# Kernel tuning notes

Hardware: AMD Instinct MI355X
Metric: run time of the kernel (lower is better)

## Reference

```python
import jax, jax.numpy as jnp
import numpy as np

DIM = 2048
NUM_SLOTS = 64
MEM_DIM = 512
TEMP = 0.1


def setup_inputs() -> dict:
    key = jax.random.key(0)
    k_x, k_mem, k_kp, k_vp, k_gw, k_gb = jax.random.split(key, 6)
    B, L = 8, 4096
    return {
        "x": jax.random.normal(k_x, (B, L, DIM), dtype=jnp.float32),
        "memory": jax.random.normal(k_mem, (NUM_SLOTS, MEM_DIM), dtype=jnp.float32),
        # torch Linear weight layout: [out_features, in_features]
        "key_w": jax.random.normal(k_kp, (MEM_DIM, DIM), dtype=jnp.float32) * (1.0 / np.sqrt(DIM)),
        "value_w": jax.random.normal(k_vp, (DIM, MEM_DIM), dtype=jnp.float32) * (1.0 / np.sqrt(MEM_DIM)),
        "gate_w": jax.random.normal(k_gw, (1, 2 * DIM), dtype=jnp.float32) * (1.0 / np.sqrt(2 * DIM)),
        "gate_b": jnp.zeros((1,), dtype=jnp.float32),
    }


def reference(x, memory, key_w, value_w, gate_w, gate_b):
    # query = key_proj(x): [B,L,mem_dim]
    query = jnp.einsum('bld,md->blm', x, key_w)
    # attention over memory slots: [B,L,num_slots]
    attn = jax.nn.softmax(jnp.einsum('blm,nm->bln', query, memory) / TEMP, axis=-1)
    # retrieve and project back to dim: [B,L,dim]
    retrieved = jnp.einsum('bln,nm->blm', attn, memory)
    retrieved = jnp.einsum('blm,dm->bld', retrieved, value_w)
    # gate from concat([x, retrieved]) -> Linear(2*dim, 1) -> sigmoid
    gate_logit = (jnp.einsum('bld,od->blo', x, gate_w[:, :DIM])
                  + jnp.einsum('bld,od->blo', retrieved, gate_w[:, DIM:])
                  + gate_b)
    gate = jax.nn.sigmoid(gate_logit)  # [B,L,1]
    return gate * x + (1.0 - gate) * retrieved
```

## Files before the change

### kernel.cpp

```cpp
#include <hip/hip_runtime.h>
#include <stdint.h>

#define DIM   2048
#define NSLOT 64
#define MDIM  512
#define TINV  10.0f

typedef __attribute__((ext_vector_type(4))) float     f32x4;
typedef __attribute__((ext_vector_type(8))) _Float16  half8;

#define MFMA16(a,b,c) __builtin_amdgcn_mfma_f32_16x16x32_f16((a),(b),(c),0,0,0)

#define OFF_W2F   0
#define OFF_W3T   1310720
#define OFF_H     1572864
#define OFF_TPART 1573120

__device__ __forceinline__ size_t w2f_idx(int row, int k, int lvl) {
    const int t  = row >> 4, ar = row & 15;
    const int ch = k >> 7, ks = (k >> 5) & 3, kg = (k >> 3) & 3, e = k & 7;
    return ((size_t)((((ch * 5 + t) * 4 + ks) * 2 + lvl) * 64) + kg * 16 + ar) * 8 + e;
}


__global__ __launch_bounds__(256) void prep_all(
    const float* __restrict__ memory, const float* __restrict__ key_w,
    const float* __restrict__ value_w, const float* __restrict__ gate_w,
    _Float16* __restrict__ W2F, _Float16* __restrict__ W3T,
    float* __restrict__ tpart)
{
    const int tid = threadIdx.x;
    const int c = blockIdx.x;
    const int role = blockIdx.y;

    if (role == 17) {
        const int b = c;
        float a0 = 0.f, a1 = 0.f;
        for (int d = b * 256; d < b * 256 + 256; ++d) {
            const float gv = gate_w[DIM + d];
            a0 = fmaf(value_w[(size_t)d * MDIM + tid], gv, a0);
            a1 = fmaf(value_w[(size_t)d * MDIM + tid + 256], gv, a1);
        }
        tpart[b * 512 + tid] = a0;
        tpart[b * 512 + tid + 256] = a1;
        return;
    }

    if (role < 9) {
        const int g = role;
        const int k = c * 256 + tid;
        if (g == 8) {
            float v = gate_w[k];
            _Float16 ph = (_Float16)v;
            _Float16 pl = (_Float16)(v - (float)ph);
            W2F[w2f_idx(64, k, 0)] = ph;
            W2F[w2f_idx(64, k, 1)] = pl;
            for (int r = 65; r < 80; ++r) {
                W2F[w2f_idx(r, k, 0)] = (_Float16)0.f;
                W2F[w2f_idx(r, k, 1)] = (_Float16)0.f;
            }
            return;
        }
        __shared__ __align__(16) float mem_s[8 * MDIM];
        for (int i = tid; i < 8 * MDIM; i += 256)
            mem_s[i] = memory[g * 8 * MDIM + i];
        __syncthreads();

        const f32x4* ms4 = (const f32x4*)mem_s;
        float acc[8] = {};
        for (int m4 = 0; m4 < MDIM / 4; ++m4) {
            const float kw0 = key_w[(size_t)(m4 * 4 + 0) * DIM + k];
            const float kw1 = key_w[(size_t)(m4 * 4 + 1) * DIM + k];
            const float kw2 = key_w[(size_t)(m4 * 4 + 2) * DIM + k];
            const float kw3 = key_w[(size_t)(m4 * 4 + 3) * DIM + k];
            #pragma unroll
            for (int i = 0; i < 8; ++i) {
                const f32x4 mv = ms4[i * (MDIM / 4) + m4];
                acc[i] = fmaf(mv.x, kw0, acc[i]);
                acc[i] = fmaf(mv.y, kw1, acc[i]);
                acc[i] = fmaf(mv.z, kw2, acc[i]);
                acc[i] = fmaf(mv.w, kw3, acc[i]);
            }
        }
        #pragma unroll
        for (int i = 0; i < 8; ++i) {
            float v = acc[i];
            _Float16 ph = (_Float16)v;
            _Float16 pl = (_Float16)(v - (float)ph);
            W2F[w2f_idx(g * 8 + i, k, 0)] = ph;
            W2F[w2f_idx(g * 8 + i, k, 1)] = pl;
        }
        return;
    }

    {
        const int g = role - 9;
        const int d = c * 256 + tid;
        __shared__ __align__(16) float mem_s2[8 * MDIM];
        for (int i = tid; i < 8 * MDIM; i += 256)
            mem_s2[i] = memory[g * 8 * MDIM + i];
        __syncthreads();

        const f32x4* ms4 = (const f32x4*)mem_s2;
        const f32x4* vp = (const f32x4*)(value_w + (size_t)d * MDIM);
        float acc[8] = {};
        for (int m4 = 0; m4 < MDIM / 4; ++m4) {
            const f32x4 v = vp[m4];
            #pragma unroll
            for (int i = 0; i < 8; ++i) {
                const f32x4 mv = ms4[i * (MDIM / 4) + m4];
                acc[i] = fmaf(mv.x, v.x, acc[i]);
                acc[i] = fmaf(mv.y, v.y, acc[i]);
                acc[i] = fmaf(mv.z, v.z, acc[i]);
                acc[i] = fmaf(mv.w, v.w, acc[i]);
            }
        }
        #pragma unroll
        for (int i = 0; i < 8; ++i)
            W3T[(size_t)d * NSLOT + g * 8 + i] = (_Float16)acc[i];
    }
}

__global__ __launch_bounds__(512) void prep_h(
    const float* __restrict__ memory, const float* __restrict__ tpart,
    float* __restrict__ h)
{
    __shared__ float ts[512];
    const int tid = threadIdx.x;
    float s = 0.f;
    #pragma unroll
    for (int b = 0; b < 8; ++b) s += tpart[b * 512 + tid];
    ts[tid] = s;
    __syncthreads();
    const int lane = tid & 63, w = tid >> 6;
    #pragma unroll
    for (int q = 0; q < 8; ++q) {
        const int n = w * 8 + q;
        float p = 0.f;
        for (int m = lane; m < MDIM; m += 64)
            p = fmaf(memory[(size_t)n * MDIM + m], ts[m], p);
        #pragma unroll
        for (int off = 32; off; off >>= 1) p += __shfl_xor(p, off);
        if (lane == 0) h[n] = p;
    }
}


__global__ __launch_bounds__(512, 4) void fused_kernel(
    const float* __restrict__ x,
    const _Float16* __restrict__ W2F,
    const _Float16* __restrict__ W3T,
    const float* __restrict__ h, const float* __restrict__ gate_b,
    float* __restrict__ out)
{
    __shared__ __align__(16) float ppart[4 * 5 * 64 * 4];
    __shared__ __align__(16) _Float16 attn_s[4][16][72];
    __shared__ float gate_s[4][16];

    const int tid  = threadIdx.x;
    const int lane = tid & 63;
    const int w    = tid >> 6;
    const int mt   = w & 3;
    const int kh   = w >> 2;
    const int arow = lane & 15;
    const int kg   = lane >> 4;
    const size_t row0 = (size_t)blockIdx.x * 64;

    f32x4 acc[5];
    {   f32x4 z = {0.f, 0.f, 0.f, 0.f};
        #pragma unroll
        for (int t = 0; t < 5; ++t) acc[t] = z; }

    const float* xrow = x + (row0 + mt * 16 + arow) * DIM + kg * 8;
    const _Float16* w2l8 = W2F + lane * 8;
    const int chbase = kh * 8;

    f32x4 xA[8], xB[8];
    auto load_x = [&](f32x4* X, int chn) {
        #pragma unroll
        for (int ks = 0; ks < 4; ++ks) {
            X[ks * 2]     = *(const f32x4*)(xrow + chn * 128 + ks * 32);
            X[ks * 2 + 1] = *(const f32x4*)(xrow + chn * 128 + ks * 32 + 4);
        }
    };
    auto compute_chunk = [&](const f32x4* X, int ch) {
        #pragma unroll
        for (int ks = 0; ks < 4; ++ks) {
            const f32x4 xa = X[ks * 2];
            const f32x4 xb = X[ks * 2 + 1];
            const float xf[8] = {xa.x, xa.y, xa.z, xa.w, xb.x, xb.y, xb.z, xb.w};
            _Float16 hh[8], ll[8];
            #pragma unroll
            for (int u = 0; u < 8; ++u) {
                hh[u] = (_Float16)xf[u];
                ll[u] = (_Float16)(xf[u] - (float)hh[u]);
            }
            const half8 ah = {hh[0], hh[1], hh[2], hh[3], hh[4], hh[5], hh[6], hh[7]};
            const half8 al = {ll[0], ll[1], ll[2], ll[3], ll[4], ll[5], ll[6], ll[7]};
            #pragma unroll
            for (int t = 0; t < 5; ++t) {
                const _Float16* p = w2l8 + (size_t)(((ch * 5 + t) * 4 + ks) * 2) * 512;
                const half8 bh = *(const half8*)p;
                const half8 bl = *(const half8*)(p + 512);
                acc[t] = MFMA16(ah, bh, acc[t]);
                acc[t] = MFMA16(al, bh, acc[t]);
                acc[t] = MFMA16(ah, bl, acc[t]);
            }
        }
    };

    load_x(xA, chbase);
    for (int cp = 0; cp < 8; cp += 2) {
        load_x(xB, chbase + cp + 1);
        compute_chunk(xA, chbase + cp);
        if (cp + 2 < 8) load_x(xA, chbase + cp + 2);
        compute_chunk(xB, chbase + cp + 1);
    }

    if (kh == 1) {
        #pragma unroll
        for (int t = 0; t < 5; ++t)
            *(f32x4*)(ppart + (size_t)((mt * 5 + t) * 64 + lane) * 4) = acc[t];
    }
    __syncthreads();

    if (kh == 0) {
        #pragma unroll
        for (int t = 0; t < 5; ++t)
            acc[t] += *(const f32x4*)(ppart + (size_t)((mt * 5 + t) * 64 + lane) * 4);

        float hl[4];
        #pragma unroll
        for (int t = 0; t < 4; ++t) hl[t] = h[t * 16 + arow];
        const float gb = gate_b[0];

        #pragma unroll
        for (int j = 0; j < 4; ++j) {
            float m = fmaxf(fmaxf(acc[0][j], acc[1][j]), fmaxf(acc[2][j], acc[3][j]));
            #pragma unroll
            for (int off = 1; off < 16; off <<= 1) m = fmaxf(m, __shfl_xor(m, off));
            float p[4];
            float sum = 0.f;
            #pragma unroll
            for (int t = 0; t < 4; ++t) { p[t] = __expf((acc[t][j] - m) * TINV); sum += p[t]; }
            #pragma unroll
            for (int off = 1; off < 16; off <<= 1) sum += __shfl_xor(sum, off);
            const float inv = 1.f / sum;
            float gp = 0.f;
            #pragma unroll
            for (int t = 0; t < 4; ++t) {
                const float a = p[t] * inv;
                attn_s[mt][kg * 4 + j][t * 16 + arow] = (_Float16)a;
                gp = fmaf(a, hl[t], gp);
            }
            #pragma unroll
            for (int off = 1; off < 16; off <<= 1) gp += __shfl_xor(gp, off);
            const float sg = __shfl(acc[4][j], lane & 48);
            if (arow == 0)
                gate_s[mt][kg * 4 + j] = 1.f / (1.f + __expf(-(sg + gp + gb)));
        }
    }
    __syncthreads();

    const size_t rbase = row0 + mt * 16;
    const half8 a0 = *(const half8*)(&attn_s[mt][arow][kg * 8]);
    const half8 a1 = *(const half8*)(&attn_s[mt][arow][kg * 8 + 32]);
    const float g = gate_s[mt][arow];

    const size_t rowoff = (rbase + arow) * DIM + kh * 1024 + kg * 4;
    const float* xp = x + rowoff;
    float* op = out + rowoff;
    const _Float16* w3base = W3T + (size_t)(kh * 1024 + arow) * NSLOT + kg * 8;

    half8 qb0[4], qb1[4];
    f32x4 qx[4];
    #pragma unroll
    for (int s = 0; s < 4; ++s) {
        const _Float16* bp = w3base + (size_t)s * 16 * NSLOT;
        qb0[s] = *(const half8*)bp;
        qb1[s] = *(const half8*)(bp + 32);
        qx[s]  = *(const f32x4*)(xp + s * 16);
    }

    #pragma unroll 4
    for (int dt = 0; dt < 64; ++dt) {
        const int s = dt & 3;
        f32x4 r = {0.f, 0.f, 0.f, 0.f};
        r = MFMA16(qb0[s], a0, r);
        r = MFMA16(qb1[s], a1, r);
        const f32x4 xv = qx[s];
        int nt = dt + 4; if (nt > 63) nt = 63;
        const _Float16* bp = w3base + (size_t)nt * 16 * NSLOT;
        qb0[s] = *(const half8*)bp;
        qb1[s] = *(const half8*)(bp + 32);
        qx[s]  = *(const f32x4*)(xp + (size_t)nt * 16);
        f32x4 o;
        o.x = fmaf(g, xv.x - r.x, r.x);
        o.y = fmaf(g, xv.y - r.y, r.y);
        o.z = fmaf(g, xv.z - r.z, r.z);
        o.w = fmaf(g, xv.w - r.w, r.w);
        *(f32x4*)(op + dt * 16) = o;
    }
}


extern "C" void kernel_launch(void* const* d_in, const int* in_sizes, int n_in,
                              void* d_out, int out_size, void* d_ws, size_t ws_size,
                              hipStream_t stream) {
    (void)in_sizes; (void)n_in; (void)out_size; (void)ws_size;
    const float* x       = (const float*)d_in[0];
    const float* memory  = (const float*)d_in[1];
    const float* key_w   = (const float*)d_in[2];
    const float* value_w = (const float*)d_in[3];
    const float* gate_w  = (const float*)d_in[4];
    const float* gate_b  = (const float*)d_in[5];
    float* out = (float*)d_out;

    char* wsb = (char*)d_ws;
    _Float16* W2F = (_Float16*)(wsb + OFF_W2F);
    _Float16* W3T = (_Float16*)(wsb + OFF_W3T);
    float*    h   = (float*)(wsb + OFF_H);
    float*    tpt = (float*)(wsb + OFF_TPART);

    prep_all<<<dim3(8, 18), 256, 0, stream>>>(memory, key_w, value_w, gate_w,
                                              W2F, W3T, tpt);
    prep_h  <<<1, 512, 0, stream>>>(memory, tpt, h);

    fused_kernel<<<512, 512, 0, stream>>>(x, W2F, W3T, h, gate_b, out);
}
```

Baseline: 301.5 us.

## Stage 16-row x panel in LDS via direct global-to-LDS loads and reuse it

The fused kernel now processes 16 rows per 256-thread block. It copies the whole 16x2048 fp32 x panel into swizzled LDS with global_load_lds, then reuses that panel for the key projection, the gate dot product with x, and the final blend, with output staged in LDS and written out coalesced. This removes the second global read of x and the fifth (gate) MFMA tile from the projection. The catch is 128KB of LDS per block, which limits occupancy to roughly one block per CU, and a four-way K split that needs a cross-warp reduction.

```diff
diff --git a/kernel.cpp b/kernel.cpp
--- a/kernel.cpp
+++ b/kernel.cpp
@@ -10,6 +10,8 @@
 typedef __attribute__((ext_vector_type(8))) _Float16  half8;
 
 #define MFMA16(a,b,c) __builtin_amdgcn_mfma_f32_16x16x32_f16((a),(b),(c),0,0,0)
+#define AS1 __attribute__((address_space(1)))
+#define AS3 __attribute__((address_space(3)))
 
 #define OFF_W2F   0
 #define OFF_W3T   1310720
@@ -18,8 +20,9 @@
 
 __device__ __forceinline__ size_t w2f_idx(int row, int k, int lvl) {
     const int t  = row >> 4, ar = row & 15;
-    const int ch = k >> 7, ks = (k >> 5) & 3, kg = (k >> 3) & 3, e = k & 7;
-    return ((size_t)((((ch * 5 + t) * 4 + ks) * 2 + lvl) * 64) + kg * 16 + ar) * 8 + e;
+    const int ch = k >> 6, ks = (k >> 5) & 1, kg = (k >> 3) & 3, e = k & 7;
+    return (size_t)ch * 12288 +
+           ((size_t)(((t * 2 + ks) * 2 + lvl) * 64) + kg * 16 + ar) * 8 + e;
 }
 
 
@@ -146,92 +149,119 @@
 }
 
 
-__global__ __launch_bounds__(512, 4) void fused_kernel(
+__global__ __launch_bounds__(256) void fused_kernel(
     const float* __restrict__ x,
     const _Float16* __restrict__ W2F,
     const _Float16* __restrict__ W3T,
-    const float* __restrict__ h, const float* __restrict__ gate_b,
-    float* __restrict__ out)
+    const float* __restrict__ h, const float* __restrict__ gate_w,
+    const float* __restrict__ gate_b, float* __restrict__ out)
 {
-    __shared__ __align__(16) float ppart[4 * 5 * 64 * 4];
-    __shared__ __align__(16) _Float16 attn_s[4][16][72];
-    __shared__ float gate_s[4][16];
+    __shared__ __align__(16) float panel[16 * 2048];
+    __shared__ __align__(16) float ppart[3 * 4 * 64 * 4];
+    __shared__ __align__(16) _Float16 attn_s[16][72];
+    __shared__ float xg[16];
+    __shared__ float gate_s[16];
 
     const int tid  = threadIdx.x;
     const int lane = tid & 63;
     const int w    = tid >> 6;
-    const int mt   = w & 3;
-    const int kh   = w >> 2;
-    const int arow = lane & 15;
+    const int ar   = lane & 15;
     const int kg   = lane >> 4;
-    const size_t row0 = (size_t)blockIdx.x * 64;
-
-    f32x4 acc[5];
+    const size_t row0 = (size_t)blockIdx.x * 16;
+
+    #pragma unroll
+    for (int i = 0; i < 32; ++i) {
+        const int g   = i * 256 + tid;
+        const int row = g >> 9, q = g & 511;
+        const int lq  = q ^ (row & 7);
+        const char* src = (const char*)x + (row0 + row) * 8192 + (size_t)lq * 16;
+        float* dst = panel + (size_t)(i * 256 + w * 64) * 4;
+        __builtin_amdgcn_global_load_lds((const AS1 void*)src, (AS3 void*)dst, 16, 0, 0);
+    }
+    asm volatile("s_waitcnt vmcnt(0)" ::: "memory");
+    __builtin_amdgcn_s_barrier();
+
+    #pragma unroll
+    for (int rr = 0; rr < 4; ++rr) {
+        const int r = w * 4 + rr;
+        float a = 0.f;
+        #pragma unroll
+        for (int j = 0; j < 32; ++j) {
+            const int d = j * 64 + lane;
+            const float f = panel[r * 2048 + (((d >> 2) ^ (r & 7)) << 2) + (d & 3)];
+            a = fmaf(f, gate_w[d], a);
+        }
+        #pragma unroll
+        for (int off = 32; off; off >>= 1) a += __shfl_xor(a, off);
+        if (lane == 0) xg[r] = a;
+    }
+
+    f32x4 acc[4];
     {   f32x4 z = {0.f, 0.f, 0.f, 0.f};
         #pragma unroll
-        for (int t = 0; t < 5; ++t) acc[t] = z; }
-
-    const float* xrow = x + (row0 + mt * 16 + arow) * DIM + kg * 8;
-    const _Float16* w2l8 = W2F + lane * 8;
-    const int chbase = kh * 8;
-
-    f32x4 xA[8], xB[8];
-    auto load_x = [&](f32x4* X, int chn) {
-        #pragma unroll
-        for (int ks = 0; ks < 4; ++ks) {
-            X[ks * 2]     = *(const f32x4*)(xrow + chn * 128 + ks * 32);
-            X[ks * 2 + 1] = *(const f32x4*)(xrow + chn * 128 + ks * 32 + 4);
-        }
+        for (int t = 0; t < 4; ++t) acc[t] = z; }
+
+    const _Float16* w2base = W2F + lane * 8;
+    auto frp = [&](int s, int t, int lvl) {
+        const int ch  = w * 8 + (s >> 1);
+        const int grp = (t * 2 + (s & 1)) * 2 + lvl;
+        return (const half8*)(w2base + (size_t)ch * 12288 + grp * 512);
     };
-    auto compute_chunk = [&](const f32x4* X, int ch) {
-        #pragma unroll
-        for (int ks = 0; ks < 4; ++ks) {
-            const f32x4 xa = X[ks * 2];
-            const f32x4 xb = X[ks * 2 + 1];
-            const float xf[8] = {xa.x, xa.y, xa.z, xa.w, xb.x, xb.y, xb.z, xb.w};
-            _Float16 hh[8], ll[8];
-            #pragma unroll
-            for (int u = 0; u < 8; ++u) {
-                hh[u] = (_Float16)xf[u];
-                ll[u] = (_Float16)(xf[u] - (float)hh[u]);
-            }
-            const half8 ah = {hh[0], hh[1], hh[2], hh[3], hh[4], hh[5], hh[6], hh[7]};
-            const half8 al = {ll[0], ll[1], ll[2], ll[3], ll[4], ll[5], ll[6], ll[7]};
-            #pragma unroll
-            for (int t = 0; t < 5; ++t) {
-                const _Float16* p = w2l8 + (size_t)(((ch * 5 + t) * 4 + ks) * 2) * 512;
-                const half8 bh = *(const half8*)p;
-                const half8 bl = *(const half8*)(p + 512);
-                acc[t] = MFMA16(ah, bh, acc[t]);
-                acc[t] = MFMA16(al, bh, acc[t]);
-                acc[t] = MFMA16(ah, bl, acc[t]);
-            }
-        }
-    };
-
-    load_x(xA, chbase);
-    for (int cp = 0; cp < 8; cp += 2) {
-        load_x(xB, chbase + cp + 1);
-        compute_chunk(xA, chbase + cp);
-        if (cp + 2 < 8) load_x(xA, chbase + cp + 2);
-        compute_chunk(xB, chbase + cp + 1);
-    }
-
-    if (kh == 1) {
-        #pragma unroll
-        for (int t = 0; t < 5; ++t)
-            *(f32x4*)(ppart + (size_t)((mt * 5 + t) * 64 + lane) * 4) = acc[t];
+
+    half8 fr[2][4][2];
+    #pragma unroll
+    for (int t = 0; t < 4; ++t) {
+        fr[0][t][0] = *frp(0, t, 0);
+        fr[0][t][1] = *frp(0, t, 1);
+    }
+
+    #pragma unroll
+    for (int s = 0; s < 16; ++s) {
+        const int cur = s & 1, nxt = cur ^ 1;
+        if (s < 15) {
+            #pragma unroll
+            for (int t = 0; t < 4; ++t) {
+                fr[nxt][t][0] = *frp(s + 1, t, 0);
+                fr[nxt][t][1] = *frp(s + 1, t, 1);
+            }
+        }
+        const int lq0 = w * 128 + s * 8 + kg * 2;
+        const f32x4 xa = *(const f32x4*)(panel + ((size_t)ar * 512 + (lq0 ^ (ar & 7))) * 4);
+        const f32x4 xb = *(const f32x4*)(panel + ((size_t)ar * 512 + ((lq0 + 1) ^ (ar & 7))) * 4);
+        const float xf[8] = {xa.x, xa.y, xa.z, xa.w, xb.x, xb.y, xb.z, xb.w};
+        _Float16 hh[8], ll[8];
+        #pragma unroll
+        for (int u = 0; u < 8; ++u) {
+            hh[u] = (_Float16)xf[u];
+            ll[u] = (_Float16)(xf[u] - (float)hh[u]);
+        }
+        const half8 ah = {hh[0], hh[1], hh[2], hh[3], hh[4], hh[5], hh[6], hh[7]};
+        const half8 al = {ll[0], ll[1], ll[2], ll[3], ll[4], ll[5], ll[6], ll[7]};
+        #pragma unroll
+        for (int t = 0; t < 4; ++t) {
+            acc[t] = MFMA16(ah, fr[cur][t][0], acc[t]);
+            acc[t] = MFMA16(al, fr[cur][t][0], acc[t]);
+            acc[t] = MFMA16(ah, fr[cur][t][1], acc[t]);
+        }
+    }
+
+    if (w > 0) {
+        #pragma unroll
+        for (int t = 0; t < 4; ++t)
+            *(f32x4*)(ppart + (size_t)(((w - 1) * 4 + t) * 64 + lane) * 4) = acc[t];
     }
     __syncthreads();
 
-    if (kh == 0) {
-        #pragma unroll
-        for (int t = 0; t < 5; ++t)
-            acc[t] += *(const f32x4*)(ppart + (size_t)((mt * 5 + t) * 64 + lane) * 4);
+    if (w == 0) {
+        #pragma unroll
+        for (int q = 0; q < 3; ++q)
+            #pragma unroll
+            for (int t = 0; t < 4; ++t)
+                acc[t] += *(const f32x4*)(ppart + (size_t)((q * 4 + t) * 64 + lane) * 4);
 
         float hl[4];
         #pragma unroll
-        for (int t = 0; t < 4; ++t) hl[t] = h[t * 16 + arow];
+        for (int t = 0; t < 4; ++t) hl[t] = h[t * 16 + ar];
         const float gb = gate_b[0];
 
         #pragma unroll
@@ -246,60 +276,65 @@
             #pragma unroll
             for (int off = 1; off < 16; off <<= 1) sum += __shfl_xor(sum, off);
             const float inv = 1.f / sum;
+            const int row = kg * 4 + j;
             float gp = 0.f;
             #pragma unroll
             for (int t = 0; t < 4; ++t) {
                 const float a = p[t] * inv;
-                attn_s[mt][kg * 4 + j][t * 16 + arow] = (_Float16)a;
+                attn_s[row][t * 16 + ar] = (_Float16)a;
                 gp = fmaf(a, hl[t], gp);
             }
             #pragma unroll
             for (int off = 1; off < 16; off <<= 1) gp += __shfl_xor(gp, off);
-            const float sg = __shfl(acc[4][j], lane & 48);
-            if (arow == 0)
-                gate_s[mt][kg * 4 + j] = 1.f / (1.f + __expf(-(sg + gp + gb)));
+            if (ar == 0)
+                gate_s[row] = 1.f / (1.f + __expf(-(xg[row] + gp + gb)));
         }
     }
     __syncthreads();
 
-    const size_t rbase = row0 + mt * 16;
-    const half8 a0 = *(const half8*)(&attn_s[mt][arow][kg * 8]);
-    const half8 a1 = *(const half8*)(&attn_s[mt][arow][kg * 8 + 32]);
-    const float g = gate_s[mt][arow];
-
-    const size_t rowoff = (rbase + arow) * DIM + kh * 1024 + kg * 4;
-    const float* xp = x + rowoff;
-    float* op = out + rowoff;
-    const _Float16* w3base = W3T + (size_t)(kh * 1024 + arow) * NSLOT + kg * 8;
+    const half8 a0 = *(const half8*)(&attn_s[ar][kg * 8]);
+    const half8 a1 = *(const half8*)(&attn_s[ar][kg * 8 + 32]);
+    const float g = gate_s[ar];
+    const _Float16* w3base = W3T + (size_t)(w * 512 + ar) * NSLOT + kg * 8;
 
     half8 qb0[4], qb1[4];
-    f32x4 qx[4];
     #pragma unroll
     for (int s = 0; s < 4; ++s) {
         const _Float16* bp = w3base + (size_t)s * 16 * NSLOT;
         qb0[s] = *(const half8*)bp;
         qb1[s] = *(const half8*)(bp + 32);
-        qx[s]  = *(const f32x4*)(xp + s * 16);
     }
 
     #pragma unroll 4
-    for (int dt = 0; dt < 64; ++dt) {
+    for (int dt = 0; dt < 32; ++dt) {
         const int s = dt & 3;
         f32x4 r = {0.f, 0.f, 0.f, 0.f};
         r = MFMA16(qb0[s], a0, r);
         r = MFMA16(qb1[s], a1, r);
-        const f32x4 xv = qx[s];
-        int nt = dt + 4; if (nt > 63) nt = 63;
+        int nt = dt + 4; if (nt > 31) nt = 31;
         const _Float16* bp = w3base + (size_t)nt * 16 * NSLOT;
         qb0[s] = *(const half8*)bp;
         qb1[s] = *(const half8*)(bp + 32);
-        qx[s]  = *(const f32x4*)(xp + (size_t)nt * 16);
+        const size_t pg = (size_t)ar * 512 + ((w * 128 + dt * 4 + kg) ^ (ar & 7));
+        const f32x4 xv = *(const f32x4*)(panel + pg * 4);
         f32x4 o;
         o.x = fmaf(g, xv.x - r.x, r.x);
         o.y = fmaf(g, xv.y - r.y, r.y);
         o.z = fmaf(g, xv.z - r.z, r.z);
         o.w = fmaf(g, xv.w - r.w, r.w);
-        *(f32x4*)(op + dt * 16) = o;
+        *(f32x4*)(panel + pg * 4) = o;
+    }
+
+    asm volatile("s_waitcnt lgkmcnt(0)" ::: "memory");
+    __builtin_amdgcn_sched_barrier(0);
+    #pragma unroll
+    for (int rr = 0; rr < 16; ++rr) {
+        #pragma unroll
+        for (int b = 0; b < 2; ++b) {
+            const int lq = w * 128 + lane * 2 + b;
+            const f32x4 v = *(const f32x4*)(panel + ((size_t)rr * 512 + (lq ^ (rr & 7))) * 4);
+            *(f32x4*)((char*)out + (row0 + rr) * 8192 + (size_t)lq * 16) = v;
+        }
     }
 }
 
@@ -326,5 +361,5 @@
                                               W2F, W3T, tpt);
     prep_h  <<<1, 512, 0, stream>>>(memory, tpt, h);
 
-    fused_kernel<<<512, 512, 0, stream>>>(x, W2F, W3T, h, gate_b, out);
-}
+    fused_kernel<<<2048, 256, 0, stream>>>(x, W2F, W3T, h, gate_w, gate_b, out);
+}
```

Result: slower. 355.8 us (+18.0%).
